# Performance work log

Measured on AMD Instinct MI355X. Metric: run time of the kernel, lower is better.

The kernel has to match this reference:

```python
import jax, jax.numpy as jnp
import numpy as np

B, C, H, W = 4, 2048, 14, 14
N_CLS, WORD_D, INT_D = 80, 300, 1024


def setup_inputs() -> dict:
    key = jax.random.key(0)
    ks = jax.random.split(key, 8)
    s = lambda fan_in: 1.0 / np.sqrt(fan_in)
    return {
        "img_feature_map": jax.random.normal(ks[0], (B, C, H, W), jnp.float32),
        "word_features": jax.random.normal(ks[1], (N_CLS, WORD_D), jnp.float32),
        "fc1_w": jax.random.uniform(ks[2], (INT_D, C), jnp.float32, -s(C), s(C)),
        "fc2_w": jax.random.uniform(ks[3], (INT_D, WORD_D), jnp.float32, -s(WORD_D), s(WORD_D)),
        "fc3_w": jax.random.uniform(ks[4], (INT_D, INT_D), jnp.float32, -s(INT_D), s(INT_D)),
        "fc3_b": jax.random.uniform(ks[5], (INT_D,), jnp.float32, -s(INT_D), s(INT_D)),
        "fc4_w": jax.random.uniform(ks[6], (1, INT_D), jnp.float32, -s(INT_D), s(INT_D)),
        "fc4_b": jax.random.uniform(ks[7], (1,), jnp.float32, -s(INT_D), s(INT_D)),
    }


def reference(img_feature_map, word_features, fc1_w, fc2_w, fc3_w, fc3_b, fc4_w, fc4_b):
    b, c, h, w = img_feature_map.shape
    n = word_features.shape[0]
    # [B,C,H,W] -> [B,H,W,C]
    x = jnp.transpose(img_feature_map, (0, 2, 3, 1))
    img_p = jnp.einsum('bhwc,dc->bhwd', x, fc1_w)            # [B,H,W,INT_D]
    word_p = word_features @ fc2_w.T                          # [N,INT_D]
    # broadcast product instead of .repeat(): [B,H,W,N,INT_D]
    feat = jnp.tanh(img_p[:, :, :, None, :] * word_p[None, None, None, :, :])
    feat = jnp.einsum('bhwnd,ed->bhwne', feat, fc3_w) + fc3_b
    coef = jnp.einsum('bhwnd,d->bhwn', feat, fc4_w[0]) + fc4_b[0]  # [B,H,W,N]
    # softmax over spatial positions per (batch, class)
    coef = jax.nn.softmax(coef.reshape(b, h * w, n), axis=1).reshape(b, h, w, n)
    # weighted spatial pooling: [B,N,C]
    return jnp.einsum('bhwn,bhwc->bnc', coef, x)
```

## Files before the change

kernel.cpp:

```cpp
#include <hip/hip_runtime.h>

typedef __attribute__((ext_vector_type(8))) short short8;
typedef __attribute__((ext_vector_type(4))) float f32x4;
typedef __attribute__((ext_vector_type(4))) unsigned short u16x4;

#define B_   4
#define C_   2048
#define HW_  196
#define P_   784
#define NCLS 80
#define WD   300
#define ID   1024

#define WP_OFF    0
#define V_OFF     81920
#define BS_OFF    82944
#define IMGP_OFF  83968
#define LG_OFF    3295232
#define VPART_OFF 3357952
#define ABF_BYTE  13748224
#define WBF_BYTE  16959488

__device__ __forceinline__ unsigned short f2bf(float x) {
    unsigned u = __float_as_uint(x);
    return (unsigned short)((u + 0x7FFFu + ((u >> 16) & 1u)) >> 16);
}

__global__ __launch_bounds__(256) void k_prep(const float* __restrict__ img,
                                              const float* __restrict__ wf,
                                              const float* __restrict__ fc1w,
                                              const float* __restrict__ fc2w,
                                              const float* __restrict__ fc3w,
                                              const float* __restrict__ fc4w,
                                              unsigned short* __restrict__ abf,
                                              unsigned short* __restrict__ wbf,
                                              float* __restrict__ wp,
                                              float* __restrict__ vpart) {
    __shared__ unsigned short tile[HW_][68];
    int bid = blockIdx.x, t = threadIdx.x;
    if (bid < 320) {
        int idx = bid * 256 + t;
        int n = idx >> 10, d = idx & 1023;
        const float4* a = (const float4*)(wf + n * WD);
        const float4* b = (const float4*)(fc2w + d * WD);
        float s = 0.f;
        #pragma unroll 5
        for (int k = 0; k < WD / 4; ++k) {
            float4 x = a[k], y = b[k];
            s += x.x * y.x + x.y * y.y + x.z * y.z + x.w * y.w;
        }
        wp[idx] = s;
    } else if (bid < 832) {
        size_t base = (size_t)(bid - 320) * 4096 + (size_t)t * 16;
        #pragma unroll
        for (int j = 0; j < 4; ++j) {
            float4 v4 = *(const float4*)(fc1w + base + j * 4);
            u16x4 r = {f2bf(v4.x), f2bf(v4.y), f2bf(v4.z), f2bf(v4.w)};
            *(u16x4*)(wbf + base + j * 4) = r;
        }
    } else if (bid < 960) {
        int bc = bid - 832;
        int c0 = (bc >> 2) * 64, b = bc & 3;
        for (int idx = t; idx < 64 * HW_; idx += 256) {
            int c = idx / HW_, hw = idx - c * HW_;
            tile[hw][c] = f2bf(img[((size_t)b * C_ + c0 + c) * HW_ + hw]);
        }
        __syncthreads();
        for (int q = t; q < 16 * HW_; q += 256) {
            int hw = q >> 4, c4 = (q & 15) * 4;
            u16x4 r = *(const u16x4*)&tile[hw][c4];
            *(u16x4*)(abf + ((size_t)b * HW_ + hw) * C_ + c0 + c4) = r;
        }
    } else {
        int idx = bid - 960;
        int ec = idx >> 2;
        int d = (idx & 3) * 256 + t;
        float s = 0.f;
        #pragma unroll 8
        for (int e = ec * 64; e < ec * 64 + 64; ++e) s += fc4w[e] * fc3w[e * ID + d];
        vpart[ec * ID + d] = s;
    }
}

#define LDT 72
__global__ __launch_bounds__(256) void k_fc1(const unsigned short* __restrict__ Abf,
                                             const unsigned short* __restrict__ Wbf,
                                             const float* __restrict__ fc3b,
                                             const float* __restrict__ fc4w,
                                             const float* __restrict__ fc4b,
                                             const float* __restrict__ vpart,
                                             float* __restrict__ imgp4,
                                             float* __restrict__ v,
                                             float* __restrict__ bs) {
    __shared__ unsigned short As[2][64 * LDT];
    __shared__ unsigned short Bs[2][64 * LDT];
    int t = threadIdx.x;
    int bx = blockIdx.x, by = blockIdx.y, bz = blockIdx.z;
    int w = t >> 6, l = t & 63;
    int lr = l & 15, lhi = l >> 4;
    int row = t >> 2, cq = (t & 3) * 16;

    int pA = bx * 64 + row;
    int pAc = pA < P_ ? pA : P_ - 1;
    const unsigned short* aBase = Abf + (size_t)pAc * C_ + bz * 512 + cq;
    const unsigned short* bBase = Wbf + (size_t)(by * 64 + row) * C_ + bz * 512 + cq;

    short8 ra0, ra1, rb0, rb1;
    f32x4 acc[4];
    #pragma unroll
    for (int j = 0; j < 4; ++j) acc[j] = (f32x4){0.f, 0.f, 0.f, 0.f};

    #define LOADR(kc) { \
        const short8* ap = (const short8*)(aBase + (kc) * 64); \
        const short8* bp = (const short8*)(bBase + (kc) * 64); \
        ra0 = ap[0]; ra1 = ap[1]; rb0 = bp[0]; rb1 = bp[1]; }
    #define WRITES(buf) { \
        *(short8*)&As[buf][row * LDT + cq]     = ra0; \
        *(short8*)&As[buf][row * LDT + cq + 8] = ra1; \
        *(short8*)&Bs[buf][row * LDT + cq]     = rb0; \
        *(short8*)&Bs[buf][row * LDT + cq + 8] = rb1; }

    LOADR(0);
    WRITES(0);
    __syncthreads();

    for (int kc = 0; kc < 8; ++kc) {
        int cur = kc & 1;
        if (kc < 7) LOADR(kc + 1);
        #pragma unroll
        for (int kk = 0; kk < 2; ++kk) {
            short8 af = *reinterpret_cast<const short8*>(
                &As[cur][(w * 16 + lr) * LDT + kk * 32 + lhi * 8]);
            #pragma unroll
            for (int j = 0; j < 4; ++j) {
                short8 bfr = *reinterpret_cast<const short8*>(
                    &Bs[cur][(j * 16 + lr) * LDT + kk * 32 + lhi * 8]);
                acc[j] = __builtin_amdgcn_mfma_f32_16x16x32_bf16(af, bfr, acc[j], 0, 0, 0);
            }
        }
        if (kc < 7) WRITES(cur ^ 1);
        __syncthreads();
    }
    #undef LOADR
    #undef WRITES

    float* outp = imgp4 + (size_t)bz * (P_ * ID);
    int prow = bx * 64 + w * 16 + lhi * 4;
    int dcol = by * 64 + lr;
    #pragma unroll
    for (int j = 0; j < 4; ++j)
        #pragma unroll
        for (int i = 0; i < 4; ++i)
            if (prow + i < P_) outp[(size_t)(prow + i) * ID + dcol + j * 16] = acc[j][i];

    if (bx == 0 && by == 0 && bz == 0) {
        for (int d = t; d < ID; d += 256) {
            float s = 0.f;
            #pragma unroll
            for (int k = 0; k < 16; ++k) s += vpart[k * ID + d];
            v[d] = s;
        }
        float s = 0.f;
        for (int i = t; i < ID; i += 256) s += fc3b[i] * fc4w[i];
        __syncthreads();
        float* red = (float*)&As[0][0];
        red[t] = s; __syncthreads();
        for (int o = 128; o > 0; o >>= 1) { if (t < o) red[t] += red[t + o]; __syncthreads(); }
        if (t == 0) bs[0] = red[0] + fc4b[0];
    }
}

__global__ __launch_bounds__(256) void k_logits(const float* __restrict__ imgp4,
                                                const float* __restrict__ wp,
                                                const float* __restrict__ v,
                                                const float* __restrict__ bs,
                                                float* __restrict__ lg) {
    __shared__ float wpl[10 * ID];
    int bx = blockIdx.x, by = blockIdx.y;
    int t = threadIdx.x, wv = t >> 6, lane = t & 63;
    int p = bx * 4 + wv;
    const int S = P_ * ID;
    const float* ap = imgp4 + (size_t)p * ID;
    const float K2 = 2.8853900817779268f;
    f32x4 a2[4], nv2[4];
    float sv = 0.f;
    #pragma unroll
    for (int q = 0; q < 4; ++q) {
        int d = q * 256 + lane * 4;
        f32x4 aq = *(const f32x4*)(ap + d);
        aq += *(const f32x4*)(ap + S + d);
        aq += *(const f32x4*)(ap + 2 * S + d);
        aq += *(const f32x4*)(ap + 3 * S + d);
        f32x4 vq = *(const f32x4*)(v + d);
        a2[q] = aq * K2;
        nv2[q] = vq * -2.0f;
        sv += vq.x + vq.y + vq.z + vq.w;
    }
    float bsv = bs[0];
    int n0 = by * 20;
    #pragma unroll
    for (int ch = 0; ch < 2; ++ch) {
        const float* src = wp + (size_t)(n0 + ch * 10) * ID;
        __syncthreads();
        #pragma unroll
        for (int k = 0; k < 10; ++k)
            *(f32x4*)(wpl + k * ID + t * 4) = *(const f32x4*)(src + k * ID + t * 4);
        __syncthreads();
        #pragma unroll 2
        for (int r = 0; r < 10; ++r) {
            float s = sv;
            #pragma unroll
            for (int q = 0; q < 4; ++q) {
                f32x4 wq = *(const f32x4*)(wpl + r * ID + q * 256 + lane * 4);
                float e0 = __builtin_amdgcn_exp2f(a2[q].x * wq.x);
                float e1 = __builtin_amdgcn_exp2f(a2[q].y * wq.y);
                float e2 = __builtin_amdgcn_exp2f(a2[q].z * wq.z);
                float e3 = __builtin_amdgcn_exp2f(a2[q].w * wq.w);
                s += nv2[q].x * __builtin_amdgcn_rcpf(e0 + 1.f);
                s += nv2[q].y * __builtin_amdgcn_rcpf(e1 + 1.f);
                s += nv2[q].z * __builtin_amdgcn_rcpf(e2 + 1.f);
                s += nv2[q].w * __builtin_amdgcn_rcpf(e3 + 1.f);
            }
            #pragma unroll
            for (int off = 32; off > 0; off >>= 1) s += __shfl_xor(s, off, 64);
            if (lane == 0) lg[p * NCLS + n0 + ch * 10 + r] = s + bsv;
        }
    }
}

__global__ __launch_bounds__(256) void k_pool(const float* __restrict__ lg,
                                              const float* __restrict__ img,
                                              float* __restrict__ out) {
    __shared__ float smt[16 * HW_];
    int cb = blockIdx.x, nt = blockIdx.y, b = blockIdx.z, t = threadIdx.x;
    int n_l = t >> 4, seg = t & 15;
    int n = nt * 16 + n_l;
    float xr[13];
    float mx = -1e30f;
    #pragma unroll
    for (int j = 0; j < 13; ++j) {
        int hw = seg + j * 16;
        float x = (hw < HW_) ? lg[(size_t)(b * HW_ + hw) * NCLS + n] : -1e30f;
        xr[j] = x; mx = fmaxf(mx, x);
    }
    #pragma unroll
    for (int o = 8; o > 0; o >>= 1) mx = fmaxf(mx, __shfl_xor(mx, o, 16));
    float sum = 0.f;
    #pragma unroll
    for (int j = 0; j < 13; ++j) {
        int hw = seg + j * 16;
        float e = (hw < HW_) ? __expf(xr[j] - mx) : 0.f;
        xr[j] = e; sum += e;
    }
    #pragma unroll
    for (int o = 8; o > 0; o >>= 1) sum += __shfl_xor(sum, o, 16);
    float inv = __builtin_amdgcn_rcpf(sum);
    #pragma unroll
    for (int j = 0; j < 13; ++j) {
        int hw = seg + j * 16;
        if (hw < HW_) smt[n_l * HW_ + hw] = xr[j] * inv;
    }
    __syncthreads();

    int c = cb * 256 + t;
    const float* row = img + ((size_t)b * C_ + c) * HW_;
    float acc[16] = {};
    for (int h4 = 0; h4 < HW_ / 4; ++h4) {
        float4 iv = *(const float4*)(row + h4 * 4);
        #pragma unroll
        for (int nl = 0; nl < 16; ++nl) {
            float4 s4 = *(const float4*)&smt[nl * HW_ + h4 * 4];
            acc[nl] += iv.x * s4.x + iv.y * s4.y + iv.z * s4.z + iv.w * s4.w;
        }
    }
    #pragma unroll
    for (int nl = 0; nl < 16; ++nl)
        out[((size_t)b * NCLS + nt * 16 + nl) * C_ + c] = acc[nl];
}

extern "C" void kernel_launch(void* const* d_in, const int* in_sizes, int n_in,
                              void* d_out, int out_size, void* d_ws, size_t ws_size,
                              hipStream_t stream) {
    const float* img  = (const float*)d_in[0];
    const float* wf   = (const float*)d_in[1];
    const float* fc1w = (const float*)d_in[2];
    const float* fc2w = (const float*)d_in[3];
    const float* fc3w = (const float*)d_in[4];
    const float* fc3b = (const float*)d_in[5];
    const float* fc4w = (const float*)d_in[6];
    const float* fc4b = (const float*)d_in[7];
    float* out = (float*)d_out;
    float* ws  = (float*)d_ws;

    float* wp    = ws + WP_OFF;
    float* v     = ws + V_OFF;
    float* bs    = ws + BS_OFF;
    float* imgp4 = ws + IMGP_OFF;
    float* lg    = ws + LG_OFF;
    float* vpart = ws + VPART_OFF;
    unsigned short* Abf = (unsigned short*)((char*)d_ws + ABF_BYTE);
    unsigned short* Wbf = (unsigned short*)((char*)d_ws + WBF_BYTE);

    k_prep   <<<dim3(1024),      256, 0, stream>>>(img, wf, fc1w, fc2w, fc3w, fc4w,
                                                   Abf, Wbf, wp, vpart);
    k_fc1    <<<dim3(13, 16, 4), 256, 0, stream>>>(Abf, Wbf, fc3b, fc4w, fc4b, vpart,
                                                   imgp4, v, bs);
    k_logits <<<dim3(196, 4),    256, 0, stream>>>(imgp4, wp, v, bs, lg);
    k_pool   <<<dim3(8, 5, 4),   256, 0, stream>>>(lg, img, out);
}
```

Baseline: 161.4 us.

## Fuse fc1 GEMM with tanh-logit epilogue, drop split-K and imgp buffer

Merges the fc1 GEMM and logit kernels: each block now runs the full K=2048 reduction and computes the tanh/fc3/fc4 contribution for its 64-column slice directly from accumulator registers, then atomically adds partial logits per class into a zeroed lg buffer. This removes the 4-way split-K fp32 imgp4 write and reread and one kernel launch. It drops the bias constant, which is softmax-invariant. The trade-off is only 208 blocks doing 4x longer K loops, plus 80 classes of atomics per block.

```diff
diff --git a/kernel.cpp b/kernel.cpp
--- a/kernel.cpp
+++ b/kernel.cpp
@@ -11,15 +11,13 @@
 #define NCLS 80
 #define WD   300
 #define ID   1024
+#define LG_N 62720
 
 #define WP_OFF    0
-#define V_OFF     81920
-#define BS_OFF    82944
-#define IMGP_OFF  83968
-#define LG_OFF    3295232
-#define VPART_OFF 3357952
-#define ABF_BYTE  13748224
-#define WBF_BYTE  16959488
+#define VPART_OFF 81920
+#define LG_OFF    98304
+#define ABF_BYTE  644096
+#define WBF_BYTE  3855360
 
 __device__ __forceinline__ unsigned short f2bf(float x) {
     unsigned u = __float_as_uint(x);
@@ -35,7 +33,8 @@
                                               unsigned short* __restrict__ abf,
                                               unsigned short* __restrict__ wbf,
                                               float* __restrict__ wp,
-                                              float* __restrict__ vpart) {
+                                              float* __restrict__ vpart,
+                                              float* __restrict__ lg) {
     __shared__ unsigned short tile[HW_][68];
     int bid = blockIdx.x, t = threadIdx.x;
     if (bid < 320) {
@@ -71,7 +70,7 @@
             u16x4 r = *(const u16x4*)&tile[hw][c4];
             *(u16x4*)(abf + ((size_t)b * HW_ + hw) * C_ + c0 + c4) = r;
         }
-    } else {
+    } else if (bid < 1024) {
         int idx = bid - 960;
         int ec = idx >> 2;
         int d = (idx & 3) * 256 + t;
@@ -79,31 +78,42 @@
         #pragma unroll 8
         for (int e = ec * 64; e < ec * 64 + 64; ++e) s += fc4w[e] * fc3w[e * ID + d];
         vpart[ec * ID + d] = s;
+    } else {
+        int base = (bid - 1024) * 1024 + t * 4;
+        if (base < LG_N) *(f32x4*)(lg + base) = (f32x4){0.f, 0.f, 0.f, 0.f};
     }
 }
 
 #define LDT 72
-__global__ __launch_bounds__(256) void k_fc1(const unsigned short* __restrict__ Abf,
-                                             const unsigned short* __restrict__ Wbf,
-                                             const float* __restrict__ fc3b,
-                                             const float* __restrict__ fc4w,
-                                             const float* __restrict__ fc4b,
-                                             const float* __restrict__ vpart,
-                                             float* __restrict__ imgp4,
-                                             float* __restrict__ v,
-                                             float* __restrict__ bs) {
-    __shared__ unsigned short As[2][64 * LDT];
-    __shared__ unsigned short Bs[2][64 * LDT];
+__global__ __launch_bounds__(256) void k_fused(const unsigned short* __restrict__ Abf,
+                                               const unsigned short* __restrict__ Wbf,
+                                               const float* __restrict__ wp,
+                                               const float* __restrict__ vpart,
+                                               float* __restrict__ lg) {
+    __shared__ char smem[36864];
+    unsigned short (*As)[64 * LDT] = (unsigned short (*)[64 * LDT])smem;
+    unsigned short (*Bs)[64 * LDT] = (unsigned short (*)[64 * LDT])(smem + 18432);
+    float* wpl = (float*)smem;
+
     int t = threadIdx.x;
-    int bx = blockIdx.x, by = blockIdx.y, bz = blockIdx.z;
+    int bx = blockIdx.x, by = blockIdx.y;
     int w = t >> 6, l = t & 63;
     int lr = l & 15, lhi = l >> 4;
     int row = t >> 2, cq = (t & 3) * 16;
 
     int pA = bx * 64 + row;
     int pAc = pA < P_ ? pA : P_ - 1;
-    const unsigned short* aBase = Abf + (size_t)pAc * C_ + bz * 512 + cq;
-    const unsigned short* bBase = Wbf + (size_t)(by * 64 + row) * C_ + bz * 512 + cq;
+    const unsigned short* aBase = Abf + (size_t)pAc * C_ + cq;
+    const unsigned short* bBase = Wbf + (size_t)(by * 64 + row) * C_ + cq;
+
+    float vj[4];
+    #pragma unroll
+    for (int j = 0; j < 4; ++j) {
+        float s = 0.f;
+        #pragma unroll
+        for (int k = 0; k < 16; ++k) s += vpart[k * ID + by * 64 + j * 16 + lr];
+        vj[j] = -2.0f * s;
+    }
 
     short8 ra0, ra1, rb0, rb1;
     f32x4 acc[4];
@@ -124,9 +134,9 @@
     WRITES(0);
     __syncthreads();
 
-    for (int kc = 0; kc < 8; ++kc) {
+    for (int kc = 0; kc < 32; ++kc) {
         int cur = kc & 1;
-        if (kc < 7) LOADR(kc + 1);
+        if (kc < 31) LOADR(kc + 1);
         #pragma unroll
         for (int kk = 0; kk < 2; ++kk) {
             short8 af = *reinterpret_cast<const short8*>(
@@ -138,93 +148,47 @@
                 acc[j] = __builtin_amdgcn_mfma_f32_16x16x32_bf16(af, bfr, acc[j], 0, 0, 0);
             }
         }
-        if (kc < 7) WRITES(cur ^ 1);
+        if (kc < 31) WRITES(cur ^ 1);
         __syncthreads();
     }
     #undef LOADR
     #undef WRITES
 
-    float* outp = imgp4 + (size_t)bz * (P_ * ID);
-    int prow = bx * 64 + w * 16 + lhi * 4;
-    int dcol = by * 64 + lr;
-    #pragma unroll
-    for (int j = 0; j < 4; ++j)
-        #pragma unroll
-        for (int i = 0; i < 4; ++i)
-            if (prow + i < P_) outp[(size_t)(prow + i) * ID + dcol + j * 16] = acc[j][i];
-
-    if (bx == 0 && by == 0 && bz == 0) {
-        for (int d = t; d < ID; d += 256) {
-            float s = 0.f;
-            #pragma unroll
-            for (int k = 0; k < 16; ++k) s += vpart[k * ID + d];
-            v[d] = s;
-        }
-        float s = 0.f;
-        for (int i = t; i < ID; i += 256) s += fc3b[i] * fc4w[i];
-        __syncthreads();
-        float* red = (float*)&As[0][0];
-        red[t] = s; __syncthreads();
-        for (int o = 128; o > 0; o >>= 1) { if (t < o) red[t] += red[t + o]; __syncthreads(); }
-        if (t == 0) bs[0] = red[0] + fc4b[0];
-    }
-}
-
-__global__ __launch_bounds__(256) void k_logits(const float* __restrict__ imgp4,
-                                                const float* __restrict__ wp,
-                                                const float* __restrict__ v,
-                                                const float* __restrict__ bs,
-                                                float* __restrict__ lg) {
-    __shared__ float wpl[10 * ID];
-    int bx = blockIdx.x, by = blockIdx.y;
-    int t = threadIdx.x, wv = t >> 6, lane = t & 63;
-    int p = bx * 4 + wv;
-    const int S = P_ * ID;
-    const float* ap = imgp4 + (size_t)p * ID;
+    for (int idx = t; idx < NCLS * 64; idx += 256) {
+        int n = idx >> 6, dl = idx & 63;
+        wpl[idx] = wp[(size_t)n * ID + by * 64 + dl];
+    }
+    __syncthreads();
+
     const float K2 = 2.8853900817779268f;
-    f32x4 a2[4], nv2[4];
-    float sv = 0.f;
-    #pragma unroll
-    for (int q = 0; q < 4; ++q) {
-        int d = q * 256 + lane * 4;
-        f32x4 aq = *(const f32x4*)(ap + d);
-        aq += *(const f32x4*)(ap + S + d);
-        aq += *(const f32x4*)(ap + 2 * S + d);
-        aq += *(const f32x4*)(ap + 3 * S + d);
-        f32x4 vq = *(const f32x4*)(v + d);
-        a2[q] = aq * K2;
-        nv2[q] = vq * -2.0f;
-        sv += vq.x + vq.y + vq.z + vq.w;
-    }
-    float bsv = bs[0];
-    int n0 = by * 20;
-    #pragma unroll
-    for (int ch = 0; ch < 2; ++ch) {
-        const float* src = wp + (size_t)(n0 + ch * 10) * ID;
-        __syncthreads();
-        #pragma unroll
-        for (int k = 0; k < 10; ++k)
-            *(f32x4*)(wpl + k * ID + t * 4) = *(const f32x4*)(src + k * ID + t * 4);
-        __syncthreads();
-        #pragma unroll 2
-        for (int r = 0; r < 10; ++r) {
-            float s = sv;
-            #pragma unroll
-            for (int q = 0; q < 4; ++q) {
-                f32x4 wq = *(const f32x4*)(wpl + r * ID + q * 256 + lane * 4);
-                float e0 = __builtin_amdgcn_exp2f(a2[q].x * wq.x);
-                float e1 = __builtin_amdgcn_exp2f(a2[q].y * wq.y);
-                float e2 = __builtin_amdgcn_exp2f(a2[q].z * wq.z);
-                float e3 = __builtin_amdgcn_exp2f(a2[q].w * wq.w);
-                s += nv2[q].x * __builtin_amdgcn_rcpf(e0 + 1.f);
-                s += nv2[q].y * __builtin_amdgcn_rcpf(e1 + 1.f);
-                s += nv2[q].z * __builtin_amdgcn_rcpf(e2 + 1.f);
-                s += nv2[q].w * __builtin_amdgcn_rcpf(e3 + 1.f);
-            }
-            #pragma unroll
-            for (int off = 32; off > 0; off >>= 1) s += __shfl_xor(s, off, 64);
-            if (lane == 0) lg[p * NCLS + n0 + ch * 10 + r] = s + bsv;
-        }
+    #pragma unroll
+    for (int j = 0; j < 4; ++j) acc[j] *= K2;
+
+    int pbase = bx * 64 + w * 16 + lhi * 4;
+    for (int n = 0; n < NCLS; ++n) {
+        float s0 = 0.f, s1 = 0.f, s2 = 0.f, s3 = 0.f;
+        #pragma unroll
+        for (int j = 0; j < 4; ++j) {
+            float wn = wpl[n * 64 + j * 16 + lr];
+            float e0 = __builtin_amdgcn_exp2f(acc[j][0] * wn);
+            float e1 = __builtin_amdgcn_exp2f(acc[j][1] * wn);
+            float e2 = __builtin_amdgcn_exp2f(acc[j][2] * wn);
+            float e3 = __builtin_amdgcn_exp2f(acc[j][3] * wn);
+            s0 += vj[j] * __builtin_amdgcn_rcpf(e0 + 1.f);
+            s1 += vj[j] * __builtin_amdgcn_rcpf(e1 + 1.f);
+            s2 += vj[j] * __builtin_amdgcn_rcpf(e2 + 1.f);
+            s3 += vj[j] * __builtin_amdgcn_rcpf(e3 + 1.f);
+        }
+        #pragma unroll
+        for (int m = 1; m < 16; m <<= 1) {
+            s0 += __shfl_xor(s0, m, 64);
+            s1 += __shfl_xor(s1, m, 64);
+            s2 += __shfl_xor(s2, m, 64);
+            s3 += __shfl_xor(s3, m, 64);
+        }
+        float sw = (lr == 0) ? s0 : (lr == 1) ? s1 : (lr == 2) ? s2 : s3;
+        int p = pbase + lr;
+        if (lr < 4 && p < P_) atomicAdd(&lg[n * P_ + p], sw);
     }
 }
 
@@ -240,7 +204,7 @@
     #pragma unroll
     for (int j = 0; j < 13; ++j) {
         int hw = seg + j * 16;
-        float x = (hw < HW_) ? lg[(size_t)(b * HW_ + hw) * NCLS + n] : -1e30f;
+        float x = (hw < HW_) ? lg[n * P_ + b * HW_ + hw] : -1e30f;
         xr[j] = x; mx = fmaxf(mx, x);
     }
     #pragma unroll
@@ -286,25 +250,18 @@
     const float* fc1w = (const float*)d_in[2];
     const float* fc2w = (const float*)d_in[3];
     const float* fc3w = (const float*)d_in[4];
-    const float* fc3b = (const float*)d_in[5];
     const float* fc4w = (const float*)d_in[6];
-    const float* fc4b = (const float*)d_in[7];
     float* out = (float*)d_out;
     float* ws  = (float*)d_ws;
 
     float* wp    = ws + WP_OFF;
-    float* v     = ws + V_OFF;
-    float* bs    = ws + BS_OFF;
-    float* imgp4 = ws + IMGP_OFF;
+    float* vpart = ws + VPART_OFF;
     float* lg    = ws + LG_OFF;
-    float* vpart = ws + VPART_OFF;
     unsigned short* Abf = (unsigned short*)((char*)d_ws + ABF_BYTE);
     unsigned short* Wbf = (unsigned short*)((char*)d_ws + WBF_BYTE);
 
-    k_prep   <<<dim3(1024),      256, 0, stream>>>(img, wf, fc1w, fc2w, fc3w, fc4w,
-                                                   Abf, Wbf, wp, vpart);
-    k_fc1    <<<dim3(13, 16, 4), 256, 0, stream>>>(Abf, Wbf, fc3b, fc4w, fc4b, vpart,
-                                                   imgp4, v, bs);
-    k_logits <<<dim3(196, 4),    256, 0, stream>>>(imgp4, wp, v, bs, lg);
-    k_pool   <<<dim3(8, 5, 4),   256, 0, stream>>>(lg, img, out);
-}
+    k_prep  <<<dim3(1086),    256, 0, stream>>>(img, wf, fc1w, fc2w, fc3w, fc4w,
+                                                Abf, Wbf, wp, vpart, lg);
+    k_fused <<<dim3(13, 16),  256, 0, stream>>>(Abf, Wbf, wp, vpart, lg);
+    k_pool  <<<dim3(8, 5, 4), 256, 0, stream>>>(lg, img, out);
+}
```

Result: slower. 179.1 us (+11.0%).
